# Kernel tuning notes

Measured on AMD Instinct MI355X. Metric: run time of the kernel, lower is better.

The kernel has to match this reference:

```python
import jax, jax.numpy as jnp
import numpy as np

B, N, IN_DIM = 2, 2048, 1024
HEADS, HEAD_DIM = 16, 64

def setup_inputs() -> dict:
    key = jax.random.key(0)
    k1, k2, k3, k4, k5 = jax.random.split(key, 5)
    s_in = 1.0 / np.sqrt(IN_DIM)
    s_h = 1.0 / np.sqrt(HEADS * HEAD_DIM)
    return {
        "x": jax.random.normal(k1, (B, N, IN_DIM), jnp.float32),
        "w_qkv": jax.random.normal(k2, (IN_DIM, 3 * HEADS * HEAD_DIM), jnp.float32) * s_in,
        "b_qkv": jax.random.normal(k3, (3 * HEADS * HEAD_DIM,), jnp.float32) * s_in,
        "w_proj": jax.random.normal(k4, (HEADS * HEAD_DIM, IN_DIM), jnp.float32) * s_h,
        "b_proj": jax.random.normal(k5, (IN_DIM,), jnp.float32) * s_h,
    }

def reference(x, w_qkv, b_qkv, w_proj, b_proj):
    b, n, _ = x.shape
    scale = HEAD_DIM ** (-0.5)
    qkv = x @ w_qkv + b_qkv                               # (B,N,3*H*D)
    # torch: reshape(B,N,H,3*D).permute(0,2,1,3) then chunk last dim into q,k,v
    qkv = qkv.reshape(b, n, HEADS, 3 * HEAD_DIM).transpose(0, 2, 1, 3)  # (B,H,N,3D)
    q, k, v = jnp.split(qkv, 3, axis=-1)                  # each (B,H,N,D)
    attn = jnp.einsum("bhqd,bhkd->bhqk", q, k) * scale    # (B,H,N,N)
    attn = jax.nn.softmax(attn, axis=-1)
    out = jnp.einsum("bhqk,bhkd->bhqd", attn, v)          # (B,H,N,D)
    out = out.transpose(0, 2, 1, 3).reshape(b, n, HEADS * HEAD_DIM)
    return out @ w_proj + b_proj
```

## Files before the change

kernel.cpp:

```cpp
#include <hip/hip_runtime.h>
#include <hip/hip_bf16.h>
#include <cstdint>
#include <cstddef>

#define BD 2
#define SEQ 2048
#define NH 16
#define HD 64
#define IND 1024
#define QKVD 3072
#define MROWS (BD * SEQ)
#define NSPLIT 2
#define TILES_PER_SPLIT (SEQ / 64 / NSPLIT)

typedef __attribute__((ext_vector_type(8))) short s8v;
typedef __attribute__((ext_vector_type(4))) short s4v;
typedef __attribute__((ext_vector_type(4))) float f4v;

__device__ __forceinline__ short f2bf(float f) {
  __hip_bfloat16 h = __float2bfloat16(f);
  return *reinterpret_cast<short*>(&h);
}

__device__ __forceinline__ void async_copy16(void* lds, const void* g) {
  __builtin_amdgcn_global_load_lds(
      (const __attribute__((address_space(1))) unsigned int*)g,
      (__attribute__((address_space(3))) unsigned int*)lds, 16, 0, 0);
}

__device__ __forceinline__ const s8v* lds_frag(const short* p, int row, int col) {
  int byte = (row << 7) + (col << 1);
  byte ^= ((row & 7) << 4);
  return (const s8v*)((const char*)p + byte);
}

__global__ void k_cast(const float* __restrict__ in, short* __restrict__ out, int n4) {
  int i = blockIdx.x * blockDim.x + threadIdx.x;
  if (i >= n4) return;
  float4 v = reinterpret_cast<const float4*>(in)[i];
  s4v o;
  o[0] = f2bf(v.x); o[1] = f2bf(v.y); o[2] = f2bf(v.z); o[3] = f2bf(v.w);
  reinterpret_cast<s4v*>(out)[i] = o;
}

__global__ void k_transpose_cast(const float* __restrict__ w, short* __restrict__ wT,
                                 int R, int C) {
  __shared__ float tile[32][33];
  int c0 = blockIdx.x * 32, r0 = blockIdx.y * 32;
  int tx = threadIdx.x, ty = threadIdx.y;
  #pragma unroll
  for (int j = 0; j < 32; j += 8)
    tile[ty + j][tx] = w[(size_t)(r0 + ty + j) * C + c0 + tx];
  __syncthreads();
  #pragma unroll
  for (int j = 0; j < 32; j += 8)
    wT[(size_t)(c0 + ty + j) * R + r0 + tx] = f2bf(tile[tx][ty + j]);
}

template <int MODE>
__global__ __launch_bounds__(256) void k_gemm(const short* __restrict__ A,
                                              const short* __restrict__ BT,
                                              const float* __restrict__ bias,
                                              short* __restrict__ obf,
                                              float* __restrict__ ofl,
                                              int Mr, int Nc, int K) {
  constexpr int BM = 128, BN = 128, BK = 32;
  __shared__ short As[BM][BK];
  __shared__ short Bs[BN][BK];
  const int rm = blockIdx.x * BM, cn = blockIdx.y * BN;
  const int t = threadIdx.x, l = t & 63;
  const int wm = (t >> 6) >> 1, wn = (t >> 6) & 1;
  const int lr = l & 15, lc = l >> 4;

  f4v acc[4][4];
  #pragma unroll
  for (int m = 0; m < 4; ++m)
    #pragma unroll
    for (int n = 0; n < 4; ++n) acc[m][n] = (f4v)0.0f;

  for (int k0 = 0; k0 < K; k0 += BK) {
    __syncthreads();
    #pragma unroll
    for (int p = 0; p < 2; ++p) {
      int c = p * 256 + t;
      async_copy16(&As[c >> 2][(c & 3) * 8],
                   &A[(size_t)(rm + (c >> 2)) * K + k0 + (c & 3) * 8]);
      async_copy16(&Bs[c >> 2][(c & 3) * 8],
                   &BT[(size_t)(cn + (c >> 2)) * K + k0 + (c & 3) * 8]);
    }
    __syncthreads();
    s8v af[4], bf[4];
    #pragma unroll
    for (int m = 0; m < 4; ++m)
      af[m] = *(const s8v*)&As[wm * 64 + m * 16 + lr][lc * 8];
    #pragma unroll
    for (int n = 0; n < 4; ++n)
      bf[n] = *(const s8v*)&Bs[wn * 64 + n * 16 + lr][lc * 8];
    #pragma unroll
    for (int m = 0; m < 4; ++m)
      #pragma unroll
      for (int n = 0; n < 4; ++n)
        acc[m][n] = __builtin_amdgcn_mfma_f32_16x16x32_bf16(af[m], bf[n], acc[m][n], 0, 0, 0);
  }

  const int row0 = rm + wm * 64, col0 = cn + wn * 64;
  #pragma unroll
  for (int n = 0; n < 4; ++n) {
    const int col = col0 + n * 16 + lr;
    const float bv = bias[col];
    if (MODE == 0) {
      const int h = col / 192, rem = col % 192;
      const int wch = rem >> 6, d = rem & 63;
      const float scale = (wch == 0) ? 0.125f : 1.0f;
      short* dst = obf + (size_t)wch * ((size_t)BD * NH * SEQ * HD);
      #pragma unroll
      for (int m = 0; m < 4; ++m)
        #pragma unroll
        for (int r = 0; r < 4; ++r) {
          const int row = row0 + m * 16 + lc * 4 + r;
          const int b = row >> 11, nn = row & (SEQ - 1);
          const short val = f2bf((acc[m][n][r] + bv) * scale);
          if (wch == 2)
            dst[((size_t)(b * NH + h) * HD + d) * SEQ + nn] = val;
          else
            dst[((size_t)(b * NH + h) * SEQ + nn) * HD + d] = val;
        }
    } else {
      #pragma unroll
      for (int m = 0; m < 4; ++m)
        #pragma unroll
        for (int r = 0; r < 4; ++r) {
          const int row = row0 + m * 16 + lc * 4 + r;
          ofl[(size_t)row * Nc + col] = acc[m][n][r] + bv;
        }
    }
  }
}

__global__ __launch_bounds__(256, 6) void k_attn(const short* __restrict__ Qw,
                                                 const short* __restrict__ Kw,
                                                 const short* __restrict__ Vt_g,
                                                 float* __restrict__ OP0,
                                                 float* __restrict__ OP1,
                                                 float* __restrict__ ML) {
  const int qb = blockIdx.x, bh = blockIdx.y, split = blockIdx.z;
  const size_t base = (size_t)bh * SEQ * HD;
  const int t = threadIdx.x, l = t & 63, w = t >> 6;
  const int lr = l & 15, lc = l >> 4;
  __shared__ short Ks[64 * 64];
  __shared__ short Vt[64 * 64];
  __shared__ short Ps[4][16 * 64];
  const int q0 = qb * 64 + w * 16;

  int ldsOff[2], kOff[2], vOff[2];
  #pragma unroll
  for (int p = 0; p < 2; ++p) {
    const int c = p * 256 + t;
    const int row = c >> 3, ch = (c & 7) ^ (row & 7);
    ldsOff[p] = c * 16;
    kOff[p] = row * HD + ch * 8;
    vOff[p] = row * SEQ + ch * 8;
  }
  const short* Kb = Kw + base;
  const short* Vb = Vt_g + base;

  s8v qf[2];
  #pragma unroll
  for (int s = 0; s < 2; ++s)
    qf[s] = *(const s8v*)&Qw[base + (size_t)(q0 + lr) * HD + s * 32 + lc * 8];

  f4v of[4];
  #pragma unroll
  for (int j = 0; j < 4; ++j) of[j] = (f4v)0.0f;
  float Mx = -3.0e38f, Ls = 0.0f;
  short* Pw = &Ps[w][0];

  for (int tt = 0; tt < TILES_PER_SPLIT; ++tt) {
    const size_t kv = (size_t)(split * TILES_PER_SPLIT + tt) * 64;
    __syncthreads();
    #pragma unroll
    for (int p = 0; p < 2; ++p)
      async_copy16((char*)Ks + ldsOff[p], Kb + kv * HD + kOff[p]);
    #pragma unroll
    for (int p = 0; p < 2; ++p)
      async_copy16((char*)Vt + ldsOff[p], Vb + kv + vOff[p]);
    __syncthreads();

    f4v st[4];
    #pragma unroll
    for (int j = 0; j < 4; ++j) st[j] = (f4v)0.0f;
    #pragma unroll
    for (int j = 0; j < 4; ++j)
      #pragma unroll
      for (int s = 0; s < 2; ++s) {
        s8v kf = *lds_frag(Ks, j * 16 + lr, s * 32 + lc * 8);
        st[j] = __builtin_amdgcn_mfma_f32_16x16x32_bf16(kf, qf[s], st[j], 0, 0, 0);
      }

    float pm = -3.0e38f;
    #pragma unroll
    for (int j = 0; j < 4; ++j)
      #pragma unroll
      for (int r = 0; r < 4; ++r) pm = fmaxf(pm, st[j][r]);
    pm = fmaxf(pm, __shfl_xor(pm, 16));
    pm = fmaxf(pm, __shfl_xor(pm, 32));
    const float Mn = fmaxf(Mx, pm);
    const float alpha = __expf(Mx - Mn);
    float rs = 0.0f;
    #pragma unroll
    for (int j = 0; j < 4; ++j) {
      s4v pk;
      #pragma unroll
      for (int r = 0; r < 4; ++r) {
        const float p = __expf(st[j][r] - Mn);
        rs += p;
        pk[r] = f2bf(p);
      }
      int byte = (lr << 7) + ((j * 16 + lc * 4) << 1);
      byte ^= ((lr & 7) << 4);
      *(s4v*)((char*)Pw + byte) = pk;
    }
    rs += __shfl_xor(rs, 16);
    rs += __shfl_xor(rs, 32);
    Ls = Ls * alpha + rs;
    Mx = Mn;

    float al[4];
    #pragma unroll
    for (int r = 0; r < 4; ++r) al[r] = __shfl(alpha, lc * 4 + r);
    #pragma unroll
    for (int jd = 0; jd < 4; ++jd)
      #pragma unroll
      for (int r = 0; r < 4; ++r) of[jd][r] *= al[r];

    asm volatile("s_waitcnt lgkmcnt(0)" ::: "memory");

    #pragma unroll
    for (int s = 0; s < 2; ++s) {
      s8v pf = *lds_frag(Pw, lr, s * 32 + lc * 8);
      #pragma unroll
      for (int jd = 0; jd < 4; ++jd) {
        s8v vf = *lds_frag(Vt, jd * 16 + lr, s * 32 + lc * 8);
        of[jd] = __builtin_amdgcn_mfma_f32_16x16x32_bf16(pf, vf, of[jd], 0, 0, 0);
      }
    }
  }

  float* OP = split ? OP1 : OP0;
  #pragma unroll
  for (int jd = 0; jd < 4; ++jd)
    #pragma unroll
    for (int r = 0; r < 4; ++r)
      OP[((size_t)bh * SEQ + q0 + lc * 4 + r) * HD + jd * 16 + lr] = of[jd][r];
  if (lc == 0) {
    float2 ml = make_float2(Mx, Ls);
    *reinterpret_cast<float2*>(
        &ML[((size_t)split * BD * NH * SEQ + (size_t)bh * SEQ + q0 + lr) * 2]) = ml;
  }
}

__global__ __launch_bounds__(256) void k_comb(const float* __restrict__ OP0,
                                              const float* __restrict__ OP1,
                                              const float* __restrict__ ML,
                                              short* __restrict__ AO) {
  const int gid = blockIdx.x * 256 + threadIdx.x;
  const int row = gid >> 2, c = gid & 3;
  const int bh = row >> 11, q = row & (SEQ - 1);
  const float2 ml1 = *reinterpret_cast<const float2*>(&ML[(size_t)row * 2]);
  const float2 ml2 = *reinterpret_cast<const float2*>(
      &ML[((size_t)BD * NH * SEQ + row) * 2]);
  const float M = fmaxf(ml1.x, ml2.x);
  const float w1 = __expf(ml1.x - M), w2 = __expf(ml2.x - M);
  const float inv = 1.0f / (w1 * ml1.y + w2 * ml2.y);
  const int b = bh >> 4, h = bh & 15;
  short* dst = &AO[((size_t)(b * SEQ + q) * (NH * HD)) + h * HD + c * 16];
  const size_t src = (size_t)row * HD + c * 16;
  #pragma unroll
  for (int i = 0; i < 4; ++i) {
    float4 a = reinterpret_cast<const float4*>(&OP0[src])[i];
    float4 bvv = reinterpret_cast<const float4*>(&OP1[src])[i];
    s4v o;
    o[0] = f2bf((w1 * a.x + w2 * bvv.x) * inv);
    o[1] = f2bf((w1 * a.y + w2 * bvv.y) * inv);
    o[2] = f2bf((w1 * a.z + w2 * bvv.z) * inv);
    o[3] = f2bf((w1 * a.w + w2 * bvv.w) * inv);
    reinterpret_cast<s4v*>(dst)[i] = o;
  }
}

extern "C" void kernel_launch(void* const* d_in, const int* in_sizes, int n_in,
                              void* d_out, int out_size, void* d_ws, size_t ws_size,
                              hipStream_t stream) {
  const float* x      = (const float*)d_in[0];
  const float* w_qkv  = (const float*)d_in[1];
  const float* b_qkv  = (const float*)d_in[2];
  const float* w_proj = (const float*)d_in[3];
  const float* b_proj = (const float*)d_in[4];
  float* out = (float*)d_out;

  char* ws = (char*)d_ws;
  short* wpT = (short*)(ws);
  short* Qw  = (short*)(ws + (2u << 20));
  short* Kw  = (short*)(ws + (10u << 20));
  short* Vtg = (short*)(ws + (18u << 20));
  short* AO  = (short*)(ws + (26u << 20));
  short* xb  = (short*)(ws + (34u << 20));
  short* wqT = (short*)(ws + (42u << 20));
  float* OP1 = (float*)(ws + (34u << 20));
  float* ML  = (float*)(ws + (50u << 20));
  float* OP0 = (float*)d_out;

  k_cast<<<(MROWS * IND / 4 + 255) / 256, 256, 0, stream>>>(x, xb, MROWS * IND / 4);
  dim3 tb(32, 8);
  k_transpose_cast<<<dim3(QKVD / 32, IND / 32), tb, 0, stream>>>(w_qkv, wqT, IND, QKVD);
  k_transpose_cast<<<dim3(IND / 32, IND / 32), tb, 0, stream>>>(w_proj, wpT, IND, IND);

  k_gemm<0><<<dim3(MROWS / 128, QKVD / 128), 256, 0, stream>>>(
      xb, wqT, b_qkv, Qw, nullptr, MROWS, QKVD, IND);
  k_attn<<<dim3(SEQ / 64, BD * NH, NSPLIT), 256, 0, stream>>>(Qw, Kw, Vtg, OP0, OP1, ML);
  k_comb<<<(BD * NH * SEQ * 4) / 256, 256, 0, stream>>>(OP0, OP1, ML, AO);
  k_gemm<1><<<dim3(MROWS / 128, IND / 128), 256, 0, stream>>>(
      AO, wpT, b_proj, nullptr, out, MROWS, IND, IND);
}
```

Baseline: 156.6 us.

## Double GEMM K-tile with swizzled LDS and add lazy softmax rescaling

The GEMM K-tile grows from 32 to 64. LDS tiles are now stored flat with an XOR swizzle on the 16-byte chunk index, so there are half as many barriers per K and fewer LDS bank conflicts when fragments are read. In the attention loop, the running max and the output rescale are only updated when some row's new max exceeds the stored max by more than 8. This skips the exp, shuffles and accumulator multiplies in most iterations, at the cost of exp values up to e^8 before normalization. The max and sum reductions are also rearranged into trees to shorten dependency chains.

```diff
diff --git a/kernel.cpp b/kernel.cpp
--- a/kernel.cpp
+++ b/kernel.cpp
@@ -64,14 +64,22 @@
                                               short* __restrict__ obf,
                                               float* __restrict__ ofl,
                                               int Mr, int Nc, int K) {
-  constexpr int BM = 128, BN = 128, BK = 32;
-  __shared__ short As[BM][BK];
-  __shared__ short Bs[BN][BK];
+  constexpr int BM = 128, BN = 128, BK = 64;
+  __shared__ short As[BM * BK];
+  __shared__ short Bs[BN * BK];
   const int rm = blockIdx.x * BM, cn = blockIdx.y * BN;
   const int t = threadIdx.x, l = t & 63;
   const int wm = (t >> 6) >> 1, wn = (t >> 6) & 1;
   const int lr = l & 15, lc = l >> 4;
 
+  int sRow[4], sCh[4];
+  #pragma unroll
+  for (int p = 0; p < 4; ++p) {
+    const int c = p * 256 + t;
+    sRow[p] = c >> 3;
+    sCh[p] = ((c & 7) ^ (sRow[p] & 7)) * 8;
+  }
+
   f4v acc[4][4];
   #pragma unroll
   for (int m = 0; m < 4; ++m)
@@ -81,26 +89,27 @@
   for (int k0 = 0; k0 < K; k0 += BK) {
     __syncthreads();
     #pragma unroll
-    for (int p = 0; p < 2; ++p) {
-      int c = p * 256 + t;
-      async_copy16(&As[c >> 2][(c & 3) * 8],
-                   &A[(size_t)(rm + (c >> 2)) * K + k0 + (c & 3) * 8]);
-      async_copy16(&Bs[c >> 2][(c & 3) * 8],
-                   &BT[(size_t)(cn + (c >> 2)) * K + k0 + (c & 3) * 8]);
+    for (int p = 0; p < 4; ++p) {
+      const int c = p * 256 + t;
+      async_copy16((char*)As + c * 16, &A[(size_t)(rm + sRow[p]) * K + k0 + sCh[p]]);
+      async_copy16((char*)Bs + c * 16, &BT[(size_t)(cn + sRow[p]) * K + k0 + sCh[p]]);
     }
     __syncthreads();
-    s8v af[4], bf[4];
-    #pragma unroll
-    for (int m = 0; m < 4; ++m)
-      af[m] = *(const s8v*)&As[wm * 64 + m * 16 + lr][lc * 8];
-    #pragma unroll
-    for (int n = 0; n < 4; ++n)
-      bf[n] = *(const s8v*)&Bs[wn * 64 + n * 16 + lr][lc * 8];
-    #pragma unroll
-    for (int m = 0; m < 4; ++m)
+    #pragma unroll
+    for (int ks = 0; ks < 2; ++ks) {
+      s8v af[4], bf[4];
+      #pragma unroll
+      for (int m = 0; m < 4; ++m)
+        af[m] = *lds_frag(As, wm * 64 + m * 16 + lr, ks * 32 + lc * 8);
       #pragma unroll
       for (int n = 0; n < 4; ++n)
-        acc[m][n] = __builtin_amdgcn_mfma_f32_16x16x32_bf16(af[m], bf[n], acc[m][n], 0, 0, 0);
+        bf[n] = *lds_frag(Bs, wn * 64 + n * 16 + lr, ks * 32 + lc * 8);
+      #pragma unroll
+      for (int m = 0; m < 4; ++m)
+        #pragma unroll
+        for (int n = 0; n < 4; ++n)
+          acc[m][n] = __builtin_amdgcn_mfma_f32_16x16x32_bf16(af[m], bf[n], acc[m][n], 0, 0, 0);
+    }
   }
 
   const int row0 = rm + wm * 64, col0 = cn + wn * 64;
@@ -197,41 +206,47 @@
         st[j] = __builtin_amdgcn_mfma_f32_16x16x32_bf16(kf, qf[s], st[j], 0, 0, 0);
       }
 
-    float pm = -3.0e38f;
+    float mj[4];
     #pragma unroll
     for (int j = 0; j < 4; ++j)
-      #pragma unroll
-      for (int r = 0; r < 4; ++r) pm = fmaxf(pm, st[j][r]);
+      mj[j] = fmaxf(fmaxf(st[j][0], st[j][1]), fmaxf(st[j][2], st[j][3]));
+    float pm = fmaxf(fmaxf(mj[0], mj[1]), fmaxf(mj[2], mj[3]));
     pm = fmaxf(pm, __shfl_xor(pm, 16));
     pm = fmaxf(pm, __shfl_xor(pm, 32));
-    const float Mn = fmaxf(Mx, pm);
-    const float alpha = __expf(Mx - Mn);
-    float rs = 0.0f;
+
+    if (!__all(pm <= Mx + 8.0f)) {
+      const float Mn = fmaxf(Mx, pm);
+      const float alpha = __expf(Mx - Mn);
+      Ls *= alpha;
+      float al[4];
+      #pragma unroll
+      for (int r = 0; r < 4; ++r) al[r] = __shfl(alpha, lc * 4 + r);
+      #pragma unroll
+      for (int jd = 0; jd < 4; ++jd)
+        #pragma unroll
+        for (int r = 0; r < 4; ++r) of[jd][r] *= al[r];
+      Mx = Mn;
+    }
+
+    float rsj[4];
     #pragma unroll
     for (int j = 0; j < 4; ++j) {
       s4v pk;
+      float pv[4];
       #pragma unroll
       for (int r = 0; r < 4; ++r) {
-        const float p = __expf(st[j][r] - Mn);
-        rs += p;
-        pk[r] = f2bf(p);
+        pv[r] = __expf(st[j][r] - Mx);
+        pk[r] = f2bf(pv[r]);
       }
+      rsj[j] = (pv[0] + pv[1]) + (pv[2] + pv[3]);
       int byte = (lr << 7) + ((j * 16 + lc * 4) << 1);
       byte ^= ((lr & 7) << 4);
       *(s4v*)((char*)Pw + byte) = pk;
     }
+    float rs = (rsj[0] + rsj[1]) + (rsj[2] + rsj[3]);
     rs += __shfl_xor(rs, 16);
     rs += __shfl_xor(rs, 32);
-    Ls = Ls * alpha + rs;
-    Mx = Mn;
-
-    float al[4];
-    #pragma unroll
-    for (int r = 0; r < 4; ++r) al[r] = __shfl(alpha, lc * 4 + r);
-    #pragma unroll
-    for (int jd = 0; jd < 4; ++jd)
-      #pragma unroll
-      for (int r = 0; r < 4; ++r) of[jd][r] *= al[r];
+    Ls += rs;
 
     asm volatile("s_waitcnt lgkmcnt(0)" ::: "memory");
 
```

Measured after the change: 145.8 us. -6.8%, faster.
